# Performance work log

Measured on AMD Instinct MI355X. Metric: run time of the kernel, lower is better.

The kernel has to match this reference:

```python
import jax, jax.numpy as jnp
import numpy as np
from functools import partial

V, CTX, D, H, L, FF = 50257, 1024, 768, 12, 12, 3072
DH = D // H
EPS = 1e-5


def _ln(x, g, b):
    m = jnp.mean(x, axis=-1, keepdims=True)
    v = jnp.mean(jnp.square(x - m), axis=-1, keepdims=True)
    return (x - m) * jax.lax.rsqrt(v + EPS) * g + b


def setup_inputs() -> dict:
    key = jax.random.key(0)
    ks = jax.random.split(key, 8)
    s = 0.02
    return {
        "input_ids": jax.random.randint(ks[0], (2, 1024), 0, V),
        "token_emb": jax.random.normal(ks[1], (V, D), jnp.float32) * s,
        "pos_emb": jax.random.normal(ks[2], (CTX, D), jnp.float32) * s,
        "ln1_g": jnp.ones((L, D), jnp.float32),
        "ln1_b": jnp.zeros((L, D), jnp.float32),
        "qkv_w": jax.random.normal(ks[3], (L, 3 * D, D), jnp.float32) * s,
        "out_w": jax.random.normal(ks[4], (L, D, D), jnp.float32) * (s / np.sqrt(2 * L)),
        "ln2_g": jnp.ones((L, D), jnp.float32),
        "ln2_b": jnp.zeros((L, D), jnp.float32),
        "ff1_w": jax.random.normal(ks[5], (L, FF, D), jnp.float32) * s,
        "ff2_w": jax.random.normal(ks[6], (L, D, FF), jnp.float32) * s,
        "lnf_g": jnp.ones((D,), jnp.float32),
        "lnf_b": jnp.zeros((D,), jnp.float32),
    }


def reference(input_ids, token_emb, pos_emb, ln1_g, ln1_b, qkv_w, out_w,
              ln2_g, ln2_b, ff1_w, ff2_w, lnf_g, lnf_b):
    B, T = input_ids.shape
    x = token_emb[input_ids] + pos_emb[:T]  # [B,T,D]
    causal = jnp.tril(jnp.ones((T, T), bool))  # True = keep
    scale = 1.0 / np.sqrt(DH)

    def block(x, p):
        g1, b1, wqkv, wo, g2, b2, w1, w2 = p
        h = _ln(x, g1, b1)
        qkv = h @ wqkv.T  # [B,T,3D]
        q, k, v = jnp.split(qkv, 3, axis=-1)
        q = q.reshape(B, T, H, DH).transpose(0, 2, 1, 3)
        k = k.reshape(B, T, H, DH).transpose(0, 2, 1, 3)
        v = v.reshape(B, T, H, DH).transpose(0, 2, 1, 3)
        scores = jnp.einsum('bhqd,bhkd->bhqk', q, k) * scale
        scores = jnp.where(causal, scores, -jnp.inf)
        w = jax.nn.softmax(scores, axis=-1)
        o = jnp.einsum('bhqk,bhkd->bhqd', w, v)
        o = o.transpose(0, 2, 1, 3).reshape(B, T, D) @ wo.T
        x = x + o
        h2 = _ln(x, g2, b2)
        ff = jax.nn.gelu(h2 @ w1.T, approximate=False) @ w2.T
        return x + ff, None

    params = (ln1_g, ln1_b, qkv_w, out_w, ln2_g, ln2_b, ff1_w, ff2_w)
    x, _ = jax.lax.scan(block, x, params)
    x = _ln(x, lnf_g, lnf_b)
    logits = x @ token_emb.T  # tied lm head
    return logits
```

## Files before the change

kernel.cpp:

```cpp
#include <hip/hip_runtime.h>
#include <hip/hip_bf16.h>
#include <math.h>

#define D_MODEL 768
#define NHEAD 12
#define DHEAD 64
#define NLAYER 12
#define FF_DIM 3072
#define SEQ 1024
#define TOKENS 2048
#define VOCAB 50257

typedef short bf16x8 __attribute__((ext_vector_type(8)));
typedef float f32x4 __attribute__((ext_vector_type(4)));
typedef unsigned short u16x4 __attribute__((ext_vector_type(4)));
typedef unsigned short u16x8 __attribute__((ext_vector_type(8)));

__device__ inline unsigned short f2bf(float f) {
    union { float f; unsigned u; } un;
    un.f = f;
    unsigned u = un.u;
    u += 0x7fffu + ((u >> 16) & 1u);
    return (unsigned short)(u >> 16);
}

__device__ inline void gl_lds16(const void* g, void* l) {
    __builtin_amdgcn_global_load_lds(
        (const __attribute__((address_space(1))) unsigned int*)g,
        (__attribute__((address_space(3))) unsigned int*)l, 16, 0, 0);
}

template<int N> __device__ __forceinline__ void waitcnt_vm() {
    static_assert(N == 0 || N == 3 || N == 4 || N == 5 || N == 6 || N == 8, "add case");
    if constexpr (N == 0) asm volatile("s_waitcnt vmcnt(0)" ::: "memory");
    else if constexpr (N == 3) asm volatile("s_waitcnt vmcnt(3)" ::: "memory");
    else if constexpr (N == 4) asm volatile("s_waitcnt vmcnt(4)" ::: "memory");
    else if constexpr (N == 5) asm volatile("s_waitcnt vmcnt(5)" ::: "memory");
    else if constexpr (N == 6) asm volatile("s_waitcnt vmcnt(6)" ::: "memory");
    else if constexpr (N == 8) asm volatile("s_waitcnt vmcnt(8)" ::: "memory");
}

__global__ __launch_bounds__(256) void cvt_kernel(const float* __restrict__ s,
                                                  unsigned short* __restrict__ d,
                                                  long n4) {
    long i = (long)blockIdx.x * 256 + threadIdx.x;
    long stride = (long)gridDim.x * 256;
    for (; i < n4; i += stride) {
        f32x4 v = ((const f32x4*)s)[i];
        u16x4 r;
        r[0] = f2bf(v[0]); r[1] = f2bf(v[1]); r[2] = f2bf(v[2]); r[3] = f2bf(v[3]);
        ((u16x4*)d)[i] = r;
    }
}

__global__ __launch_bounds__(256) void embed_kernel(const int* __restrict__ ids,
                                                    const float* __restrict__ tok,
                                                    const float* __restrict__ pos,
                                                    float* __restrict__ x) {
    int i = blockIdx.x * 256 + threadIdx.x;
    int row = i / D_MODEL;
    int d = i - row * D_MODEL;
    int t = row & (SEQ - 1);
    x[i] = tok[(long)ids[row] * D_MODEL + d] + pos[(long)t * D_MODEL + d];
}

__global__ __launch_bounds__(256) void ln_kernel(const float* __restrict__ x,
                                                 const float* __restrict__ g,
                                                 const float* __restrict__ b,
                                                 unsigned short* __restrict__ out) {
    int row = blockIdx.x;
    int tid = threadIdx.x;
    const float* xr = x + (long)row * D_MODEL;
    float v0 = xr[tid], v1 = xr[tid + 256], v2 = xr[tid + 512];
    __shared__ float sm[4];
    float s = v0 + v1 + v2;
    #pragma unroll
    for (int off = 32; off; off >>= 1) s += __shfl_xor(s, off);
    if ((tid & 63) == 0) sm[tid >> 6] = s;
    __syncthreads();
    float mean = (sm[0] + sm[1] + sm[2] + sm[3]) * (1.f / D_MODEL);
    __syncthreads();
    float d0 = v0 - mean, d1 = v1 - mean, d2 = v2 - mean;
    s = d0 * d0 + d1 * d1 + d2 * d2;
    #pragma unroll
    for (int off = 32; off; off >>= 1) s += __shfl_xor(s, off);
    if ((tid & 63) == 0) sm[tid >> 6] = s;
    __syncthreads();
    float var = (sm[0] + sm[1] + sm[2] + sm[3]) * (1.f / D_MODEL);
    float rs = rsqrtf(var + 1e-5f);
    unsigned short* orow = out + (long)row * D_MODEL;
    orow[tid]       = f2bf(d0 * rs * g[tid]       + b[tid]);
    orow[tid + 256] = f2bf(d1 * rs * g[tid + 256] + b[tid + 256]);
    orow[tid + 512] = f2bf(d2 * rs * g[tid + 512] + b[tid + 512]);
}

#define GM_NONE 0
#define GM_RES  1
#define GM_GELU 2
#define GM_QKV  3

template<int WM, int WN, int MODE, int DB>
__global__ __launch_bounds__(256) void gemm_bf16(
        const unsigned short* __restrict__ A, const unsigned short* __restrict__ W,
        int M, int N, int K,
        float* __restrict__ Cf, unsigned short* __restrict__ Cb,
        const float* __restrict__ RES,
        unsigned short* __restrict__ P1, unsigned short* __restrict__ P2) {
    constexpr int BM = WM * 32, BN = WN * 32;
    constexpr int NLD = BM / 32 + BN / 32;
    __shared__ unsigned short lA[DB][BM * 64];
    __shared__ unsigned short lB[DB][BN * 64];

    int tid = threadIdx.x;
    int lane = tid & 63, wv = tid >> 6;
    int wr = wv >> 1, wc = wv & 1;
    int lr = lane & 15, kq = lane >> 4;
    int row0 = blockIdx.x * BM;
    int col0 = blockIdx.y * BN;

    int srow_in = tid >> 3;
    int ssp = tid & 7;
    int skg = ssp ^ (srow_in & 7);
    int lbase = ((tid & ~63)) << 3;

    f32x4 acc[WM][WN];
    #pragma unroll
    for (int m = 0; m < WM; m++)
        #pragma unroll
        for (int n = 0; n < WN; n++) acc[m][n] = (f32x4){0.f, 0.f, 0.f, 0.f};

    auto stage = [&](int buf, int kt) {
        #pragma unroll
        for (int i = 0; i < BM / 32; i++) {
            int row = i * 32 + srow_in;
            gl_lds16(A + (size_t)(row0 + row) * K + kt + skg * 8,
                     &lA[buf][i * 2048 + lbase]);
        }
        #pragma unroll
        for (int i = 0; i < BN / 32; i++) {
            int row = i * 32 + srow_in;
            int srow = col0 + row;
            if (srow >= N) srow = N - 1;
            gl_lds16(W + (size_t)srow * K + kt + skg * 8,
                     &lB[buf][i * 2048 + lbase]);
        }
    };
    auto compute = [&](int buf) {
        #pragma unroll
        for (int kk = 0; kk < 2; kk++) {
            int kg = kk * 4 + kq;
            bf16x8 af[WM], bfr[WN];
            #pragma unroll
            for (int m = 0; m < WM; m++) {
                int row = wr * (WM * 16) + m * 16 + lr;
                af[m] = *(const bf16x8*)&lA[buf][row * 64 + ((kg ^ (row & 7)) << 3)];
            }
            #pragma unroll
            for (int n = 0; n < WN; n++) {
                int row = wc * (WN * 16) + n * 16 + lr;
                bfr[n] = *(const bf16x8*)&lB[buf][row * 64 + ((kg ^ (row & 7)) << 3)];
            }
            #pragma unroll
            for (int m = 0; m < WM; m++)
                #pragma unroll
                for (int n = 0; n < WN; n++)
                    acc[m][n] = __builtin_amdgcn_mfma_f32_16x16x32_bf16(af[m], bfr[n], acc[m][n], 0, 0, 0);
        }
    };

    if (DB == 2) {
        stage(0, 0);
        __builtin_amdgcn_sched_barrier(0);
        int nt = K >> 6;
        int cur = 0;
        for (int t = 0; t < nt; t++) {
            if (t + 1 < nt) {
                stage(cur ^ 1, (t + 1) << 6);
                __builtin_amdgcn_sched_barrier(0);
                waitcnt_vm<NLD>();
            } else {
                waitcnt_vm<0>();
            }
            __builtin_amdgcn_s_barrier();
            __builtin_amdgcn_sched_barrier(0);
            compute(cur);
            __builtin_amdgcn_sched_barrier(0);
            __builtin_amdgcn_s_barrier();
            cur ^= 1;
        }
    } else {
        for (int kt = 0; kt < K; kt += 64) {
            stage(0, kt);
            __syncthreads();
            compute(0);
            __syncthreads();
        }
    }

    #pragma unroll
    for (int m = 0; m < WM; m++) {
        int r0 = row0 + wr * (WM * 16) + m * 16 + (kq << 2);
        #pragma unroll
        for (int n = 0; n < WN; n++) {
            int c = col0 + wc * (WN * 16) + n * 16 + lr;
            if (c < N) {
                if (MODE == GM_QKV) {
                    int bb = r0 >> 10, t0q = r0 & 1023;
                    if (c < D_MODEL) {
                        int h = c >> 6, dh = c & 63;
                        size_t base = (((size_t)(bb * NHEAD + h) * SEQ) + t0q) * 64 + dh;
                        #pragma unroll
                        for (int j = 0; j < 4; j++)
                            P1[base + (size_t)j * 64] = f2bf(acc[m][n][j] * 0.125f);
                    } else if (c < 2 * D_MODEL) {
                        int cc = c - D_MODEL;
                        int h = cc >> 6, dh = cc & 63;
                        size_t base = (((size_t)(bb * NHEAD + h) * SEQ) + t0q) * 64 + dh;
                        #pragma unroll
                        for (int j = 0; j < 4; j++)
                            P2[base + (size_t)j * 64] = f2bf(acc[m][n][j]);
                    } else {
                        int cc = c - 2 * D_MODEL;
                        int h = cc >> 6, dh = cc & 63;
                        u16x4 vv;
                        #pragma unroll
                        for (int j = 0; j < 4; j++) vv[j] = f2bf(acc[m][n][j]);
                        *(u16x4*)(Cb + ((size_t)(bb * NHEAD + h) * 64 + dh) * SEQ + t0q) = vv;
                    }
                } else {
                    #pragma unroll
                    for (int j = 0; j < 4; j++) {
                        int r = r0 + j;
                        size_t idx = (size_t)r * N + c;
                        float v = acc[m][n][j];
                        if (MODE == GM_RES) {
                            Cf[idx] = v + RES[idx];
                        } else if (MODE == GM_GELU) {
                            Cb[idx] = f2bf(0.5f * v * (1.f + erff(v * 0.70710678118f)));
                        } else {
                            Cf[idx] = v;
                        }
                    }
                }
            }
        }
    }
}

__global__ __launch_bounds__(512, 2) void gemm256_bf16(
        const unsigned short* __restrict__ A, const unsigned short* __restrict__ W,
        int M, int N, int K, float* __restrict__ Cf) {
    __shared__ unsigned short lA[2][256 * 64];
    __shared__ unsigned short lB[2][256 * 64];

    int tid = threadIdx.x;
    int lane = tid & 63, wv = tid >> 6;
    int wr = wv >> 2, wc = wv & 3;
    int lr = lane & 15, kq = lane >> 4;
    int row0 = blockIdx.x * 256;
    int col0 = blockIdx.y * 256;

    int srow_in = tid >> 3;
    int skg = (tid & 7) ^ (srow_in & 7);
    int lbase = (tid & ~63) << 3;

    f32x4 acc[8][4];
    #pragma unroll
    for (int m = 0; m < 8; m++)
        #pragma unroll
        for (int n = 0; n < 4; n++) acc[m][n] = (f32x4){0.f, 0.f, 0.f, 0.f};

    auto stage = [&](int buf, int kt) {
        #pragma unroll
        for (int i = 0; i < 4; i++) {
            int row = i * 64 + srow_in;
            gl_lds16(A + (size_t)(row0 + row) * K + kt + skg * 8,
                     &lA[buf][i * 4096 + lbase]);
        }
        #pragma unroll
        for (int i = 0; i < 4; i++) {
            int row = i * 64 + srow_in;
            int srow = col0 + row;
            if (srow >= N) srow = N - 1;
            gl_lds16(W + (size_t)srow * K + kt + skg * 8,
                     &lB[buf][i * 4096 + lbase]);
        }
    };
    auto compute = [&](int buf) {
        #pragma unroll
        for (int kk = 0; kk < 2; kk++) {
            int kg = kk * 4 + kq;
            bf16x8 af[8], bfr[4];
            #pragma unroll
            for (int m = 0; m < 8; m++) {
                int row = wr * 128 + m * 16 + lr;
                af[m] = *(const bf16x8*)&lA[buf][row * 64 + ((kg ^ (row & 7)) << 3)];
            }
            #pragma unroll
            for (int n = 0; n < 4; n++) {
                int row = wc * 64 + n * 16 + lr;
                bfr[n] = *(const bf16x8*)&lB[buf][row * 64 + ((kg ^ (row & 7)) << 3)];
            }
            #pragma unroll
            for (int m = 0; m < 8; m++)
                #pragma unroll
                for (int n = 0; n < 4; n++)
                    acc[m][n] = __builtin_amdgcn_mfma_f32_16x16x32_bf16(af[m], bfr[n], acc[m][n], 0, 0, 0);
        }
    };

    stage(0, 0);
    __builtin_amdgcn_sched_barrier(0);
    int nt = K >> 6;
    int cur = 0;
    for (int t = 0; t < nt; t++) {
        if (t + 1 < nt) {
            stage(cur ^ 1, (t + 1) << 6);
            __builtin_amdgcn_sched_barrier(0);
            waitcnt_vm<8>();
        } else {
            waitcnt_vm<0>();
        }
        __builtin_amdgcn_s_barrier();
        __builtin_amdgcn_sched_barrier(0);
        compute(cur);
        __builtin_amdgcn_sched_barrier(0);
        __builtin_amdgcn_s_barrier();
        cur ^= 1;
    }

    #pragma unroll
    for (int m = 0; m < 8; m++) {
        int r0 = row0 + wr * 128 + m * 16 + (kq << 2);
        #pragma unroll
        for (int n = 0; n < 4; n++) {
            int c = col0 + wc * 64 + n * 16 + lr;
            if (c < N) {
                #pragma unroll
                for (int j = 0; j < 4; j++)
                    Cf[(size_t)(r0 + j) * N + c] = acc[m][n][j];
            }
        }
    }
}

#define ANW 4
__global__ __launch_bounds__(256) void attn_mfma(const unsigned short* __restrict__ Qb,
                                                 const unsigned short* __restrict__ Kb,
                                                 const unsigned short* __restrict__ Vt,
                                                 unsigned short* __restrict__ att) {
    int b = blockIdx.z, h = blockIdx.y, pr = blockIdx.x;
    int tid = threadIdx.x, l = tid & 63, w = tid >> 6;
    int lr = l & 15, hg = l >> 4;
    int hk8 = hg * 8, hg4 = hg * 4;
    size_t bh = (size_t)b * NHEAD + h;
    const unsigned short* Qp = Qb + bh * SEQ * 64;
    const unsigned short* Kp = Kb + bh * SEQ * 64;
    const unsigned short* Vp = Vt + bh * 64 * SEQ;

    __shared__ float sm_m[ANW][2][16], sm_l[ANW][2][16];
    __shared__ float sm_o[ANW][2][16][65];
    __shared__ unsigned short pl[ANW][1024];
    unsigned short* Pw = &pl[w][0];

    #pragma unroll
    for (int ti = 0; ti < 2; ti++) {
        int tile = ti ? (63 - pr) : pr;
        int q0 = tile * 16;
        bf16x8 qf0 = *(const bf16x8*)(Qp + (size_t)(q0 + lr) * 64 + hk8);
        bf16x8 qf1 = *(const bf16x8*)(Qp + (size_t)(q0 + lr) * 64 + 32 + hk8);
        f32x4 O[4];
        #pragma unroll
        for (int dt = 0; dt < 4; dt++) O[dt] = (f32x4){0.f, 0.f, 0.f, 0.f};
        f32x4 mrun = (f32x4){-1e30f, -1e30f, -1e30f, -1e30f};
        f32x4 lrun = (f32x4){0.f, 0.f, 0.f, 0.f};
        int nch = (tile >> 2) + 1;

        bf16x8 kfa[8];
        if (w < nch) {
            int k0p = w * 64;
            #pragma unroll
            for (int kt = 0; kt < 4; kt++) {
                kfa[2 * kt]     = *(const bf16x8*)(Kp + (size_t)(k0p + kt * 16 + lr) * 64 + hk8);
                kfa[2 * kt + 1] = *(const bf16x8*)(Kp + (size_t)(k0p + kt * 16 + lr) * 64 + 32 + hk8);
            }
        }

        for (int c = w; c < nch; c += ANW) {
            int k0 = c * 64;
            f32x4 S[4];
            #pragma unroll
            for (int kt = 0; kt < 4; kt++) {
                S[kt] = (f32x4){0.f, 0.f, 0.f, 0.f};
                S[kt] = __builtin_amdgcn_mfma_f32_16x16x32_bf16(qf0, kfa[2 * kt], S[kt], 0, 0, 0);
                S[kt] = __builtin_amdgcn_mfma_f32_16x16x32_bf16(qf1, kfa[2 * kt + 1], S[kt], 0, 0, 0);
            }
            bf16x8 kfb[8];
            int cn = c + ANW;
            if (cn < nch) {
                int k0n = cn * 64;
                #pragma unroll
                for (int kt = 0; kt < 4; kt++) {
                    kfb[2 * kt]     = *(const bf16x8*)(Kp + (size_t)(k0n + kt * 16 + lr) * 64 + hk8);
                    kfb[2 * kt + 1] = *(const bf16x8*)(Kp + (size_t)(k0n + kt * 16 + lr) * 64 + 32 + hk8);
                }
            }
            if (c == nch - 1) {
                #pragma unroll
                for (int kt = 0; kt < 4; kt++)
                    #pragma unroll
                    for (int j = 0; j < 4; j++)
                        S[kt][j] = (k0 + kt * 16 + lr <= q0 + hg4 + j) ? S[kt][j] : -3.0e38f;
            }
            f32x4 rm;
            #pragma unroll
            for (int j = 0; j < 4; j++)
                rm[j] = fmaxf(fmaxf(S[0][j], S[1][j]), fmaxf(S[2][j], S[3][j]));
            #pragma unroll
            for (int msk = 1; msk <= 8; msk <<= 1)
                #pragma unroll
                for (int j = 0; j < 4; j++)
                    rm[j] = fmaxf(rm[j], __shfl_xor(rm[j], msk));
            f32x4 mn, corr, rs;
            #pragma unroll
            for (int j = 0; j < 4; j++) {
                mn[j] = fmaxf(mrun[j], rm[j]);
                corr[j] = __expf(mrun[j] - mn[j]);
                rs[j] = 0.f;
            }
            #pragma unroll
            for (int kt = 0; kt < 4; kt++)
                #pragma unroll
                for (int j = 0; j < 4; j++) {
                    float p = __expf(S[kt][j] - mn[j]);
                    S[kt][j] = p;
                    rs[j] += p;
                }
            #pragma unroll
            for (int msk = 1; msk <= 8; msk <<= 1)
                #pragma unroll
                for (int j = 0; j < 4; j++)
                    rs[j] += __shfl_xor(rs[j], msk);
            #pragma unroll
            for (int j = 0; j < 4; j++) {
                lrun[j] = lrun[j] * corr[j] + rs[j];
                mrun[j] = mn[j];
            }
            #pragma unroll
            for (int dt = 0; dt < 4; dt++)
                #pragma unroll
                for (int j = 0; j < 4; j++) O[dt][j] *= corr[j];
            bf16x8 vfr[8];
            #pragma unroll
            for (int dt = 0; dt < 4; dt++) {
                vfr[2 * dt]     = *(const bf16x8*)(Vp + (size_t)(dt * 16 + lr) * SEQ + k0 + hk8);
                vfr[2 * dt + 1] = *(const bf16x8*)(Vp + (size_t)(dt * 16 + lr) * SEQ + k0 + 32 + hk8);
            }
            #pragma unroll
            for (int kt = 0; kt < 4; kt++) {
                int cc = kt * 16 + lr;
                int slot = cc >> 3, off = cc & 7;
                #pragma unroll
                for (int j = 0; j < 4; j++) {
                    int r = hg4 + j;
                    Pw[r * 64 + ((slot ^ (r & 7)) << 3) + off] = f2bf(S[kt][j]);
                }
            }
            asm volatile("s_waitcnt lgkmcnt(0)" ::: "memory");
            bf16x8 pf0 = *(const bf16x8*)&Pw[lr * 64 + ((hg ^ (lr & 7)) << 3)];
            bf16x8 pf1 = *(const bf16x8*)&Pw[lr * 64 + (((4 + hg) ^ (lr & 7)) << 3)];
            #pragma unroll
            for (int dt = 0; dt < 4; dt++) {
                O[dt] = __builtin_amdgcn_mfma_f32_16x16x32_bf16(pf0, vfr[2 * dt], O[dt], 0, 0, 0);
                O[dt] = __builtin_amdgcn_mfma_f32_16x16x32_bf16(pf1, vfr[2 * dt + 1], O[dt], 0, 0, 0);
            }
            #pragma unroll
            for (int i = 0; i < 8; i++) kfa[i] = kfb[i];
        }
        if (lr == 0) {
            #pragma unroll
            for (int j = 0; j < 4; j++) {
                sm_m[w][ti][hg4 + j] = mrun[j];
                sm_l[w][ti][hg4 + j] = lrun[j];
            }
        }
        #pragma unroll
        for (int dt = 0; dt < 4; dt++)
            #pragma unroll
            for (int j = 0; j < 4; j++)
                sm_o[w][ti][hg4 + j][dt * 16 + lr] = O[dt][j];
    }
    __syncthreads();
    {
        int ti2 = w >> 1;
        int tile = ti2 ? (63 - pr) : pr;
        int q0 = tile * 16;
        #pragma unroll
        for (int jj = 0; jj < 2; jj++) {
            int j = (w & 1) * 2 + jj;
            int r = hg4 + j;
            float m0 = sm_m[0][ti2][r], m1 = sm_m[1][ti2][r];
            float m2 = sm_m[2][ti2][r], m3 = sm_m[3][ti2][r];
            float M = fmaxf(fmaxf(m0, m1), fmaxf(m2, m3));
            float e0 = __expf(m0 - M), e1 = __expf(m1 - M);
            float e2 = __expf(m2 - M), e3 = __expf(m3 - M);
            float L = sm_l[0][ti2][r] * e0 + sm_l[1][ti2][r] * e1
                    + sm_l[2][ti2][r] * e2 + sm_l[3][ti2][r] * e3;
            float invL = 1.f / L;
            unsigned short* orow = att + ((size_t)(b * SEQ + q0 + r)) * D_MODEL + h * 64;
            #pragma unroll
            for (int dt = 0; dt < 4; dt++) {
                int cidx = dt * 16 + lr;
                float o = sm_o[0][ti2][r][cidx] * e0 + sm_o[1][ti2][r][cidx] * e1
                        + sm_o[2][ti2][r][cidx] * e2 + sm_o[3][ti2][r][cidx] * e3;
                orow[cidx] = f2bf(o * invL);
            }
        }
    }
}

extern "C" void kernel_launch(void* const* d_in, const int* in_sizes, int n_in,
                              void* d_out, int out_size, void* d_ws, size_t ws_size,
                              hipStream_t stream) {
    const int*   input_ids = (const int*)d_in[0];
    const float* token_emb = (const float*)d_in[1];
    const float* pos_emb   = (const float*)d_in[2];
    const float* ln1_g     = (const float*)d_in[3];
    const float* ln1_b     = (const float*)d_in[4];
    const float* qkv_w     = (const float*)d_in[5];
    const float* out_w     = (const float*)d_in[6];
    const float* ln2_g     = (const float*)d_in[7];
    const float* ln2_b     = (const float*)d_in[8];
    const float* ff1_w     = (const float*)d_in[9];
    const float* ff2_w     = (const float*)d_in[10];
    const float* lnf_g     = (const float*)d_in[11];
    const float* lnf_b     = (const float*)d_in[12];
    float* out = (float*)d_out;

    const size_t SZ_QKV_L = (size_t)3 * D_MODEL * D_MODEL;
    const size_t SZ_OUT_L = (size_t)D_MODEL * D_MODEL;
    const size_t SZ_FF1_L = (size_t)FF_DIM * D_MODEL;
    const size_t SZ_FF2_L = (size_t)D_MODEL * FF_DIM;
    const size_t SZ_TOK   = (size_t)VOCAB * D_MODEL;

    char* base = (char*)d_ws;
    size_t off = 0;
    auto alloc = [&](size_t bytes) -> char* {
        char* p = base + off;
        off = (off + bytes + 255) & ~(size_t)255;
        return p;
    };

    float* x              = (float*)alloc((size_t)TOKENS * D_MODEL * 4);
    unsigned short* hb    = (unsigned short*)alloc((size_t)TOKENS * D_MODEL * 2);
    unsigned short* attb  = (unsigned short*)alloc((size_t)TOKENS * D_MODEL * 2);
    unsigned short* ffab  = (unsigned short*)alloc((size_t)TOKENS * FF_DIM * 2);
    unsigned short* Qb    = (unsigned short*)alloc((size_t)TOKENS * D_MODEL * 2);
    unsigned short* Kb    = (unsigned short*)alloc((size_t)TOKENS * D_MODEL * 2);
    unsigned short* Vtb   = (unsigned short*)alloc((size_t)TOKENS * D_MODEL * 2);

    size_t act_end = off;
    size_t full_need = act_end + 2 * (NLAYER * (SZ_QKV_L + SZ_OUT_L + SZ_FF1_L + SZ_FF2_L) + SZ_TOK)
                       + 6 * 256;
    bool full = ws_size >= full_need;

    unsigned short *qkvA, *outA, *ff1A, *ff2A, *tokA;
    if (full) {
        qkvA = (unsigned short*)alloc(2 * NLAYER * SZ_QKV_L);
        outA = (unsigned short*)alloc(2 * NLAYER * SZ_OUT_L);
        ff1A = (unsigned short*)alloc(2 * NLAYER * SZ_FF1_L);
        ff2A = (unsigned short*)alloc(2 * NLAYER * SZ_FF2_L);
        tokA = (unsigned short*)alloc(2 * SZ_TOK);
    } else {
        qkvA = (unsigned short*)alloc(2 * SZ_QKV_L);
        outA = (unsigned short*)alloc(2 * SZ_OUT_L);
        ff1A = (unsigned short*)alloc(2 * SZ_FF1_L);
        ff2A = (unsigned short*)alloc(2 * SZ_FF2_L);
        tokA = (unsigned short*)alloc(2 * SZ_TOK);
    }

    auto cvt = [&](const float* s, unsigned short* d, size_t n) {
        long n4 = (long)(n / 4);
        int g = (int)((n4 + 255) / 256);
        if (g > 2048) g = 2048;
        cvt_kernel<<<g, 256, 0, stream>>>(s, d, n4);
    };

    if (full) {
        cvt(qkv_w, qkvA, NLAYER * SZ_QKV_L);
        cvt(out_w, outA, NLAYER * SZ_OUT_L);
        cvt(ff1_w, ff1A, NLAYER * SZ_FF1_L);
        cvt(ff2_w, ff2A, NLAYER * SZ_FF2_L);
        cvt(token_emb, tokA, SZ_TOK);
    }

    embed_kernel<<<TOKENS * D_MODEL / 256, 256, 0, stream>>>(input_ids, token_emb, pos_emb, x);

    for (int l = 0; l < NLAYER; l++) {
        const unsigned short* qw = full ? qkvA + (size_t)l * SZ_QKV_L : qkvA;
        const unsigned short* ow = full ? outA + (size_t)l * SZ_OUT_L : outA;
        const unsigned short* f1 = full ? ff1A + (size_t)l * SZ_FF1_L : ff1A;
        const unsigned short* f2 = full ? ff2A + (size_t)l * SZ_FF2_L : ff2A;

        ln_kernel<<<TOKENS, 256, 0, stream>>>(x, ln1_g + l * D_MODEL, ln1_b + l * D_MODEL, hb);
        if (!full) cvt(qkv_w + (size_t)l * SZ_QKV_L, qkvA, SZ_QKV_L);
        gemm_bf16<2, 3, GM_QKV, 2><<<dim3(TOKENS / 64, 3 * D_MODEL / 96), 256, 0, stream>>>(
            hb, qw, TOKENS, 3 * D_MODEL, D_MODEL, nullptr, Vtb, nullptr, Qb, Kb);
        attn_mfma<<<dim3(32, NHEAD, 2), 256, 0, stream>>>(Qb, Kb, Vtb, attb);
        if (!full) cvt(out_w + (size_t)l * SZ_OUT_L, outA, SZ_OUT_L);
        gemm_bf16<1, 2, GM_RES, 2><<<dim3(TOKENS / 32, D_MODEL / 64), 256, 0, stream>>>(
            attb, ow, TOKENS, D_MODEL, D_MODEL, x, nullptr, x, nullptr, nullptr);
        ln_kernel<<<TOKENS, 256, 0, stream>>>(x, ln2_g + l * D_MODEL, ln2_b + l * D_MODEL, hb);
        if (!full) cvt(ff1_w + (size_t)l * SZ_FF1_L, ff1A, SZ_FF1_L);
        gemm_bf16<2, 4, GM_GELU, 2><<<dim3(TOKENS / 64, FF_DIM / 128), 256, 0, stream>>>(
            hb, f1, TOKENS, FF_DIM, D_MODEL, nullptr, ffab, nullptr, nullptr, nullptr);
        if (!full) cvt(ff2_w + (size_t)l * SZ_FF2_L, ff2A, SZ_FF2_L);
        gemm_bf16<1, 2, GM_RES, 2><<<dim3(TOKENS / 32, D_MODEL / 64), 256, 0, stream>>>(
            ffab, f2, TOKENS, D_MODEL, FF_DIM, x, nullptr, x, nullptr, nullptr);
    }

    ln_kernel<<<TOKENS, 256, 0, stream>>>(x, lnf_g, lnf_b, hb);
    if (!full) cvt(token_emb, tokA, SZ_TOK);
    gemm256_bf16<<<dim3(TOKENS / 256, (VOCAB + 255) / 256), 512, 0, stream>>>(
        hb, tokA, TOKENS, VOCAB, D_MODEL, out);
}
```

Baseline: 1.987 ms.

## Share K/V chunk loads between paired low and high query tiles in attention

The attention kernel now processes its two causal query tiles (pr and 63-pr) in a single pass over key chunks instead of two sequential passes. Each K and V chunk is loaded once and used for the high tile, and also for the low tile while the chunk lies within its causal range. This cuts the global K/V loads for the low tile and gives the MFMA units more independent work per loaded chunk. In exchange it keeps two sets of accumulators and softmax state live, which raises register pressure and may lower occupancy.

```diff
diff --git a/kernel.cpp b/kernel.cpp
--- a/kernel.cpp
+++ b/kernel.cpp
@@ -363,55 +363,65 @@
     __shared__ unsigned short pl[ANW][1024];
     unsigned short* Pw = &pl[w][0];
 
+    int tlo = pr, thi = 63 - pr;
+    int q0lo = tlo * 16, q0hi = thi * 16;
+    int nlo = (tlo >> 2) + 1, nhi = (thi >> 2) + 1;
+
+    bf16x8 qlo0 = *(const bf16x8*)(Qp + (size_t)(q0lo + lr) * 64 + hk8);
+    bf16x8 qlo1 = *(const bf16x8*)(Qp + (size_t)(q0lo + lr) * 64 + 32 + hk8);
+    bf16x8 qhi0 = *(const bf16x8*)(Qp + (size_t)(q0hi + lr) * 64 + hk8);
+    bf16x8 qhi1 = *(const bf16x8*)(Qp + (size_t)(q0hi + lr) * 64 + 32 + hk8);
+
+    f32x4 Olo[4], Ohi[4];
     #pragma unroll
-    for (int ti = 0; ti < 2; ti++) {
-        int tile = ti ? (63 - pr) : pr;
-        int q0 = tile * 16;
-        bf16x8 qf0 = *(const bf16x8*)(Qp + (size_t)(q0 + lr) * 64 + hk8);
-        bf16x8 qf1 = *(const bf16x8*)(Qp + (size_t)(q0 + lr) * 64 + 32 + hk8);
-        f32x4 O[4];
-        #pragma unroll
-        for (int dt = 0; dt < 4; dt++) O[dt] = (f32x4){0.f, 0.f, 0.f, 0.f};
-        f32x4 mrun = (f32x4){-1e30f, -1e30f, -1e30f, -1e30f};
-        f32x4 lrun = (f32x4){0.f, 0.f, 0.f, 0.f};
-        int nch = (tile >> 2) + 1;
-
-        bf16x8 kfa[8];
-        if (w < nch) {
-            int k0p = w * 64;
+    for (int dt = 0; dt < 4; dt++) { Olo[dt] = (f32x4){0,0,0,0}; Ohi[dt] = (f32x4){0,0,0,0}; }
+    f32x4 mlo = (f32x4){-1e30f,-1e30f,-1e30f,-1e30f}, llo = (f32x4){0,0,0,0};
+    f32x4 mhi = mlo, lhi = llo;
+
+    bf16x8 kfa[8];
+    {
+        int k0p = w * 64;
+        #pragma unroll
+        for (int kt = 0; kt < 4; kt++) {
+            kfa[2 * kt]     = *(const bf16x8*)(Kp + (size_t)(k0p + kt * 16 + lr) * 64 + hk8);
+            kfa[2 * kt + 1] = *(const bf16x8*)(Kp + (size_t)(k0p + kt * 16 + lr) * 64 + 32 + hk8);
+        }
+    }
+
+    for (int c = w; c < nhi; c += ANW) {
+        int k0 = c * 64;
+        bool dolo = (c < nlo);
+        f32x4 S[4];
+        #pragma unroll
+        for (int kt = 0; kt < 4; kt++) {
+            S[kt] = (f32x4){0,0,0,0};
+            S[kt] = __builtin_amdgcn_mfma_f32_16x16x32_bf16(qhi0, kfa[2 * kt], S[kt], 0, 0, 0);
+            S[kt] = __builtin_amdgcn_mfma_f32_16x16x32_bf16(qhi1, kfa[2 * kt + 1], S[kt], 0, 0, 0);
+        }
+        bf16x8 kfb[8];
+        int cn = c + ANW;
+        if (cn < nhi) {
+            int k0n = cn * 64;
             #pragma unroll
             for (int kt = 0; kt < 4; kt++) {
-                kfa[2 * kt]     = *(const bf16x8*)(Kp + (size_t)(k0p + kt * 16 + lr) * 64 + hk8);
-                kfa[2 * kt + 1] = *(const bf16x8*)(Kp + (size_t)(k0p + kt * 16 + lr) * 64 + 32 + hk8);
-            }
-        }
-
-        for (int c = w; c < nch; c += ANW) {
-            int k0 = c * 64;
-            f32x4 S[4];
-            #pragma unroll
-            for (int kt = 0; kt < 4; kt++) {
-                S[kt] = (f32x4){0.f, 0.f, 0.f, 0.f};
-                S[kt] = __builtin_amdgcn_mfma_f32_16x16x32_bf16(qf0, kfa[2 * kt], S[kt], 0, 0, 0);
-                S[kt] = __builtin_amdgcn_mfma_f32_16x16x32_bf16(qf1, kfa[2 * kt + 1], S[kt], 0, 0, 0);
-            }
-            bf16x8 kfb[8];
-            int cn = c + ANW;
-            if (cn < nch) {
-                int k0n = cn * 64;
-                #pragma unroll
-                for (int kt = 0; kt < 4; kt++) {
-                    kfb[2 * kt]     = *(const bf16x8*)(Kp + (size_t)(k0n + kt * 16 + lr) * 64 + hk8);
-                    kfb[2 * kt + 1] = *(const bf16x8*)(Kp + (size_t)(k0n + kt * 16 + lr) * 64 + 32 + hk8);
-                }
-            }
-            if (c == nch - 1) {
-                #pragma unroll
-                for (int kt = 0; kt < 4; kt++)
-                    #pragma unroll
-                    for (int j = 0; j < 4; j++)
-                        S[kt][j] = (k0 + kt * 16 + lr <= q0 + hg4 + j) ? S[kt][j] : -3.0e38f;
-            }
+                kfb[2 * kt]     = *(const bf16x8*)(Kp + (size_t)(k0n + kt * 16 + lr) * 64 + hk8);
+                kfb[2 * kt + 1] = *(const bf16x8*)(Kp + (size_t)(k0n + kt * 16 + lr) * 64 + 32 + hk8);
+            }
+        }
+        bf16x8 vfr[8];
+        #pragma unroll
+        for (int dt = 0; dt < 4; dt++) {
+            vfr[2 * dt]     = *(const bf16x8*)(Vp + (size_t)(dt * 16 + lr) * SEQ + k0 + hk8);
+            vfr[2 * dt + 1] = *(const bf16x8*)(Vp + (size_t)(dt * 16 + lr) * SEQ + k0 + 32 + hk8);
+        }
+        if (c == nhi - 1) {
+            #pragma unroll
+            for (int kt = 0; kt < 4; kt++)
+                #pragma unroll
+                for (int j = 0; j < 4; j++)
+                    S[kt][j] = (k0 + kt * 16 + lr <= q0hi + hg4 + j) ? S[kt][j] : -3.0e38f;
+        }
+        {
             f32x4 rm;
             #pragma unroll
             for (int j = 0; j < 4; j++)
@@ -424,8 +434,8 @@
             f32x4 mn, corr, rs;
             #pragma unroll
             for (int j = 0; j < 4; j++) {
-                mn[j] = fmaxf(mrun[j], rm[j]);
-                corr[j] = __expf(mrun[j] - mn[j]);
+                mn[j] = fmaxf(mhi[j], rm[j]);
+                corr[j] = __expf(mhi[j] - mn[j]);
                 rs[j] = 0.f;
             }
             #pragma unroll
@@ -443,19 +453,13 @@
                     rs[j] += __shfl_xor(rs[j], msk);
             #pragma unroll
             for (int j = 0; j < 4; j++) {
-                lrun[j] = lrun[j] * corr[j] + rs[j];
-                mrun[j] = mn[j];
+                lhi[j] = lhi[j] * corr[j] + rs[j];
+                mhi[j] = mn[j];
             }
             #pragma unroll
             for (int dt = 0; dt < 4; dt++)
                 #pragma unroll
-                for (int j = 0; j < 4; j++) O[dt][j] *= corr[j];
-            bf16x8 vfr[8];
-            #pragma unroll
-            for (int dt = 0; dt < 4; dt++) {
-                vfr[2 * dt]     = *(const bf16x8*)(Vp + (size_t)(dt * 16 + lr) * SEQ + k0 + hk8);
-                vfr[2 * dt + 1] = *(const bf16x8*)(Vp + (size_t)(dt * 16 + lr) * SEQ + k0 + 32 + hk8);
-            }
+                for (int j = 0; j < 4; j++) Ohi[dt][j] *= corr[j];
             #pragma unroll
             for (int kt = 0; kt < 4; kt++) {
                 int cc = kt * 16 + lr;
@@ -471,25 +475,101 @@
             bf16x8 pf1 = *(const bf16x8*)&Pw[lr * 64 + (((4 + hg) ^ (lr & 7)) << 3)];
             #pragma unroll
             for (int dt = 0; dt < 4; dt++) {
-                O[dt] = __builtin_amdgcn_mfma_f32_16x16x32_bf16(pf0, vfr[2 * dt], O[dt], 0, 0, 0);
-                O[dt] = __builtin_amdgcn_mfma_f32_16x16x32_bf16(pf1, vfr[2 * dt + 1], O[dt], 0, 0, 0);
-            }
-            #pragma unroll
-            for (int i = 0; i < 8; i++) kfa[i] = kfb[i];
-        }
-        if (lr == 0) {
+                Ohi[dt] = __builtin_amdgcn_mfma_f32_16x16x32_bf16(pf0, vfr[2 * dt], Ohi[dt], 0, 0, 0);
+                Ohi[dt] = __builtin_amdgcn_mfma_f32_16x16x32_bf16(pf1, vfr[2 * dt + 1], Ohi[dt], 0, 0, 0);
+            }
+        }
+        if (dolo) {
+            #pragma unroll
+            for (int kt = 0; kt < 4; kt++) {
+                S[kt] = (f32x4){0,0,0,0};
+                S[kt] = __builtin_amdgcn_mfma_f32_16x16x32_bf16(qlo0, kfa[2 * kt], S[kt], 0, 0, 0);
+                S[kt] = __builtin_amdgcn_mfma_f32_16x16x32_bf16(qlo1, kfa[2 * kt + 1], S[kt], 0, 0, 0);
+            }
+            if (c == nlo - 1) {
+                #pragma unroll
+                for (int kt = 0; kt < 4; kt++)
+                    #pragma unroll
+                    for (int j = 0; j < 4; j++)
+                        S[kt][j] = (k0 + kt * 16 + lr <= q0lo + hg4 + j) ? S[kt][j] : -3.0e38f;
+            }
+            f32x4 rm;
+            #pragma unroll
+            for (int j = 0; j < 4; j++)
+                rm[j] = fmaxf(fmaxf(S[0][j], S[1][j]), fmaxf(S[2][j], S[3][j]));
+            #pragma unroll
+            for (int msk = 1; msk <= 8; msk <<= 1)
+                #pragma unroll
+                for (int j = 0; j < 4; j++)
+                    rm[j] = fmaxf(rm[j], __shfl_xor(rm[j], msk));
+            f32x4 mn, corr, rs;
             #pragma unroll
             for (int j = 0; j < 4; j++) {
-                sm_m[w][ti][hg4 + j] = mrun[j];
-                sm_l[w][ti][hg4 + j] = lrun[j];
-            }
-        }
-        #pragma unroll
-        for (int dt = 0; dt < 4; dt++)
-            #pragma unroll
-            for (int j = 0; j < 4; j++)
-                sm_o[w][ti][hg4 + j][dt * 16 + lr] = O[dt][j];
-    }
+                mn[j] = fmaxf(mlo[j], rm[j]);
+                corr[j] = __expf(mlo[j] - mn[j]);
+                rs[j] = 0.f;
+            }
+            #pragma unroll
+            for (int kt = 0; kt < 4; kt++)
+                #pragma unroll
+                for (int j = 0; j < 4; j++) {
+                    float p = __expf(S[kt][j] - mn[j]);
+                    S[kt][j] = p;
+                    rs[j] += p;
+                }
+            #pragma unroll
+            for (int msk = 1; msk <= 8; msk <<= 1)
+                #pragma unroll
+                for (int j = 0; j < 4; j++)
+                    rs[j] += __shfl_xor(rs[j], msk);
+            #pragma unroll
+            for (int j = 0; j < 4; j++) {
+                llo[j] = llo[j] * corr[j] + rs[j];
+                mlo[j] = mn[j];
+            }
+            #pragma unroll
+            for (int dt = 0; dt < 4; dt++)
+                #pragma unroll
+                for (int j = 0; j < 4; j++) Olo[dt][j] *= corr[j];
+            #pragma unroll
+            for (int kt = 0; kt < 4; kt++) {
+                int cc = kt * 16 + lr;
+                int slot = cc >> 3, off = cc & 7;
+                #pragma unroll
+                for (int j = 0; j < 4; j++) {
+                    int r = hg4 + j;
+                    Pw[r * 64 + ((slot ^ (r & 7)) << 3) + off] = f2bf(S[kt][j]);
+                }
+            }
+            asm volatile("s_waitcnt lgkmcnt(0)" ::: "memory");
+            bf16x8 pf0 = *(const bf16x8*)&Pw[lr * 64 + ((hg ^ (lr & 7)) << 3)];
+            bf16x8 pf1 = *(const bf16x8*)&Pw[lr * 64 + (((4 + hg) ^ (lr & 7)) << 3)];
+            #pragma unroll
+            for (int dt = 0; dt < 4; dt++) {
+                Olo[dt] = __builtin_amdgcn_mfma_f32_16x16x32_bf16(pf0, vfr[2 * dt], Olo[dt], 0, 0, 0);
+                Olo[dt] = __builtin_amdgcn_mfma_f32_16x16x32_bf16(pf1, vfr[2 * dt + 1], Olo[dt], 0, 0, 0);
+            }
+        }
+        #pragma unroll
+        for (int i = 0; i < 8; i++) kfa[i] = kfb[i];
+    }
+
+    if (lr == 0) {
+        #pragma unroll
+        for (int j = 0; j < 4; j++) {
+            sm_m[w][0][hg4 + j] = mlo[j];
+            sm_l[w][0][hg4 + j] = llo[j];
+            sm_m[w][1][hg4 + j] = mhi[j];
+            sm_l[w][1][hg4 + j] = lhi[j];
+        }
+    }
+    #pragma unroll
+    for (int dt = 0; dt < 4; dt++)
+        #pragma unroll
+        for (int j = 0; j < 4; j++) {
+            sm_o[w][0][hg4 + j][dt * 16 + lr] = Olo[dt][j];
+            sm_o[w][1][hg4 + j][dt * 16 + lr] = Ohi[dt][j];
+        }
     __syncthreads();
     {
         int ti2 = w >> 1;
```

Result: no change. 1.999 ms (+0.6%).
